# Kernel optimization log

Hardware: AMD Instinct MI355X
Metric: run time of the kernel (lower is better)

Reference implementation:

```python
import jax, jax.numpy as jnp
import numpy as np

B, N, K = 4, 4096, 16
D_POINTS, D_MODEL = 64, 128


def setup_inputs() -> dict:
    key = jax.random.key(0)
    ks = jax.random.split(key, 18)
    rn = lambda k, shp, s=0.05: (jax.random.normal(k, shp, jnp.float32) * s)
    return {
        "xyz": jax.random.normal(ks[0], (B, N, 3), jnp.float32),
        "features": jax.random.normal(ks[1], (B, N, D_POINTS), jnp.float32),
        # fc_delta: Linear(3,d_model) -> ReLU -> Linear(d_model,d_model)
        "Wd1": rn(ks[2], (3, D_MODEL)), "bd1": rn(ks[3], (D_MODEL,)),
        "Wd2": rn(ks[4], (D_MODEL, D_MODEL)), "bd2": rn(ks[5], (D_MODEL,)),
        # fc1: Linear(d_points, d_model)
        "Wf1": rn(ks[6], (D_POINTS, D_MODEL)), "bf1": rn(ks[7], (D_MODEL,)),
        # w_qs / w_ks / w_vs: Linear(d_model, d_model, bias=False)
        "Wq": rn(ks[8], (D_MODEL, D_MODEL)),
        "Wk": rn(ks[9], (D_MODEL, D_MODEL)),
        "Wv": rn(ks[10], (D_MODEL, D_MODEL)),
        # fc_gamma: Linear(d_model,d_model) -> ReLU -> Linear(d_model,d_model)
        "Wg1": rn(ks[11], (D_MODEL, D_MODEL)), "bg1": rn(ks[12], (D_MODEL,)),
        "Wg2": rn(ks[13], (D_MODEL, D_MODEL)), "bg2": rn(ks[14], (D_MODEL,)),
        # fc2: Linear(d_model, d_points)
        "Wo": rn(ks[15], (D_MODEL, D_POINTS)), "bo": rn(ks[16], (D_POINTS,)),
    }


def reference(xyz, features, Wd1, bd1, Wd2, bd2, Wf1, bf1, Wq, Wk, Wv,
              Wg1, bg1, Wg2, bg2, Wo, bo):
    sq = jnp.sum(xyz * xyz, axis=-1)
    d2 = sq[:, :, None] + sq[:, None, :] - 2.0 * jnp.einsum('bnd,bmd->bnm', xyz, xyz)
    # argsort()[:, :, :k] == k smallest distances (self included)
    _, knn_idx = jax.lax.top_k(-d2, K)  # [B,N,K] int32

    gather = jax.vmap(lambda a, i: a[i])  # per-batch fancy gather along point axis
    knn_xyz = gather(xyz, knn_idx)                       # [B,N,K,3]
    rel = xyz[:, :, None, :] - knn_xyz                   # [B,N,K,3]
    pos_enc = jax.nn.relu(rel @ Wd1 + bd1) @ Wd2 + bd2   # [B,N,K,D]

    shortcut = features
    f = features @ Wf1 + bf1                             # [B,N,D]
    knn_f = gather(f, knn_idx)                           # [B,N,K,D]

    q = f @ Wq                                           # [B,N,D]
    k = knn_f @ Wk                                       # [B,N,K,D]
    v = knn_f @ Wv                                       # [B,N,K,D]

    attn = q[:, :, None, :] - k + pos_enc                # [B,N,K,D]
    attn = jax.nn.relu(attn @ Wg1 + bg1) @ Wg2 + bg2
    attn = jax.nn.softmax(attn / np.sqrt(D_MODEL).astype(np.float32), axis=-2)

    res = jnp.einsum('bnkf,bnkf->bnf', attn, v + pos_enc)  # [B,N,D]
    return res @ Wo + bo + shortcut                        # [B,N,d_points]
```

## Files before the change

kernel.cpp:

```cpp
#include <hip/hip_runtime.h>
#include <hip/hip_bf16.h>

#define NPTS 4096
#define BATCH 4
#define BN (BATCH * NPTS)
#define DMODEL 128
#define DPTS 64
#define KNBR 16
#define SWS 136
#define PBLK 8

typedef unsigned short u16;
typedef unsigned int u32;
typedef unsigned long long u64;
typedef short bh8 __attribute__((ext_vector_type(8)));
typedef float f32x4 __attribute__((ext_vector_type(4)));

__device__ __forceinline__ float bfu(u16 u) {
    union { u32 i; float f; } c; c.i = ((u32)u) << 16; return c.f;
}
__device__ __forceinline__ u16 f2u(float x) {
    u32 u = __float_as_uint(x);
    u32 r = u + 0x7FFFu + ((u >> 16) & 1u);
    return (u16)(r >> 16);
}
__device__ __forceinline__ u32 pack2(float a, float b) {
    return (u32)f2u(a) | ((u32)f2u(b) << 16);
}
__device__ __forceinline__ float ldr(const void* p, long i, int mode) {
    return mode == 0 ? bfu(((const u16*)p)[i]) : ((const float*)p)[i];
}
__device__ __forceinline__ void str(void* p, long i, float v, int mode) {
    if (mode == 0) ((u16*)p)[i] = f2u(v);
    else ((float*)p)[i] = v;
}
__device__ __forceinline__ int detect_mode(const void* Wq) {
    const u16* w = (const u16*)Wq;
    int lane = threadIdx.x & 63;
    int tot = 0;
#pragma unroll
    for (int r = 0; r < 4; ++r) {
        unsigned e = (w[lane + r * 64] >> 7) & 0xFFu;
        bool wild = (e >= 132u) || (e > 0u && e <= 90u);
        tot += (int)__popcll(__ballot(wild));
    }
    return tot > 32 ? 1 : 0;
}

__global__ __launch_bounds__(256) void prep_kernel(
    const void* __restrict__ Wd2, const void* __restrict__ Wg1, const void* __restrict__ Wg2,
    const void* __restrict__ Wo, const void* __restrict__ Wq, const void* __restrict__ Wk,
    const void* __restrict__ Wv, const void* __restrict__ Wf1, const void* __restrict__ xyz,
    u16* __restrict__ WdT2, u16* __restrict__ WgT1, u16* __restrict__ WgT2,
    u16* __restrict__ WoT, u16* __restrict__ WqT, u16* __restrict__ WkT,
    u16* __restrict__ WvT, u16* __restrict__ WfT, float4* __restrict__ cloudF) {
    int mode = detect_mode(Wq);
    int gid = blockIdx.x * 256 + threadIdx.x;
    if (gid < 6 * 16384) {
        int m = gid >> 14, o = gid & 16383;
        int n = o >> 7, i = o & 127;
        const void* W = (m == 0) ? Wd2 : (m == 1) ? Wg1 : (m == 2) ? Wg2
                      : (m == 3) ? Wq  : (m == 4) ? Wk  : Wv;
        u16* D = (m == 0) ? WdT2 : (m == 1) ? WgT1 : (m == 2) ? WgT2
               : (m == 3) ? WqT  : (m == 4) ? WkT  : WvT;
        D[o] = f2u(ldr(W, (long)i * 128 + n, mode));
    } else if (gid < 6 * 16384 + 8192) {
        int o = gid - 6 * 16384;
        int n = o >> 6, k2 = o & 63;
        WfT[o] = f2u(ldr(Wf1, (long)k2 * 128 + n, mode));
    } else if (gid < 6 * 16384 + 16384) {
        int o2 = gid - 6 * 16384 - 8192;
        int col = o2 >> 7, i = o2 & 127;
        WoT[o2] = f2u(ldr(Wo, (long)i * 64 + col, mode));
    } else if (gid < 6 * 16384 + 16384 + 16384) {
        int i = gid - (6 * 16384 + 16384);
        float gx = ldr(xyz, (long)i * 3 + 0, mode);
        float gy = ldr(xyz, (long)i * 3 + 1, mode);
        float gz = ldr(xyz, (long)i * 3 + 2, mode);
        float4 f;
        f.x = gx; f.y = gy; f.z = gz;
        f.w = gx * gx + gy * gy + gz * gz;
        cloudF[i] = f;
    }
}

__global__ __launch_bounds__(256) void qkv_kernel(
    const void* __restrict__ feat, const void* __restrict__ bf1v, const void* __restrict__ WqRaw,
    const u16* __restrict__ WfT, const u16* __restrict__ WqT,
    const u16* __restrict__ WkT, const u16* __restrict__ WvT,
    u16* __restrict__ qw, u16* __restrict__ kfw, u16* __restrict__ vfw) {
    int mode = detect_mode(WqRaw);
    __shared__ __align__(16) u16 sFeat[64 * 72];
    __shared__ __align__(16) u16 sF[64 * SWS];
    const int t = threadIdx.x;
    const int p0 = blockIdx.x * 64;
    const int lane = t & 63, w = t >> 6;
    const int rg = (w & 1) * 32, cg = (w >> 1) * 64;
    const int lm = lane & 15, lq = lane >> 4;

    for (int i = t; i < 512; i += 256) {
        int r = i >> 3, c8 = i & 7;
        u16 tmp[8];
        if (mode == 0) {
            *(uint4*)tmp = *((const uint4*)feat + (long)(p0 + r) * 8 + c8);
        } else {
            const float* fp = (const float*)feat + (long)(p0 + r) * 64 + c8 * 8;
#pragma unroll
            for (int u = 0; u < 8; ++u) tmp[u] = f2u(fp[u]);
        }
        *(uint4*)(sFeat + r * 72 + c8 * 8) = *(uint4*)tmp;
    }
    __syncthreads();

    {
        f32x4 acc[2][4];
#pragma unroll
        for (int rt = 0; rt < 2; ++rt)
#pragma unroll
            for (int ct = 0; ct < 4; ++ct) { acc[rt][ct][0]=0.f; acc[rt][ct][1]=0.f; acc[rt][ct][2]=0.f; acc[rt][ct][3]=0.f; }
#pragma unroll
        for (int kk = 0; kk < 2; ++kk) {
            const int ko = kk * 32 + lq * 8;
            bh8 a0 = *(const bh8*)(sFeat + (rg + lm) * 72 + ko);
            bh8 a1 = *(const bh8*)(sFeat + (rg + 16 + lm) * 72 + ko);
            bh8 bq[4];
#pragma unroll
            for (int ct = 0; ct < 4; ++ct)
                bq[ct] = *(const bh8*)(WfT + (long)(cg + ct * 16 + lm) * 64 + ko);
#pragma unroll
            for (int ct = 0; ct < 4; ++ct) {
                acc[0][ct] = __builtin_amdgcn_mfma_f32_16x16x32_bf16(a0, bq[ct], acc[0][ct], 0, 0, 0);
                acc[1][ct] = __builtin_amdgcn_mfma_f32_16x16x32_bf16(a1, bq[ct], acc[1][ct], 0, 0, 0);
            }
        }
#pragma unroll
        for (int rt = 0; rt < 2; ++rt)
#pragma unroll
            for (int ct = 0; ct < 4; ++ct) {
                const int col = cg + ct * 16 + lm;
                const float bj = ldr(bf1v, col, mode);
#pragma unroll
                for (int r4 = 0; r4 < 4; ++r4) {
                    int row = rg + rt * 16 + lq * 4 + r4;
                    u32 u = (u32)f2u(acc[rt][ct][r4] + bj);
                    u32 o = __shfl_xor(u, 1);
                    if ((lane & 1) == 0)
                        *(u32*)(sF + row * SWS + col) = u | (o << 16);
                }
            }
    }
    __syncthreads();

    {
        const int m = blockIdx.y;
        const u16* Wm = (m == 0) ? WqT : (m == 1) ? WkT : WvT;
        u16* Om = (m == 0) ? qw : (m == 1) ? kfw : vfw;
        f32x4 acc[2][4];
#pragma unroll
        for (int rt = 0; rt < 2; ++rt)
#pragma unroll
            for (int ct = 0; ct < 4; ++ct) { acc[rt][ct][0]=0.f; acc[rt][ct][1]=0.f; acc[rt][ct][2]=0.f; acc[rt][ct][3]=0.f; }
#pragma unroll
        for (int kk = 0; kk < 4; ++kk) {
            const int ko = kk * 32 + lq * 8;
            bh8 a0 = *(const bh8*)(sF + (rg + lm) * SWS + ko);
            bh8 a1 = *(const bh8*)(sF + (rg + 16 + lm) * SWS + ko);
            bh8 bq[4];
#pragma unroll
            for (int ct = 0; ct < 4; ++ct)
                bq[ct] = *(const bh8*)(Wm + (long)(cg + ct * 16 + lm) * 128 + ko);
#pragma unroll
            for (int ct = 0; ct < 4; ++ct) {
                acc[0][ct] = __builtin_amdgcn_mfma_f32_16x16x32_bf16(a0, bq[ct], acc[0][ct], 0, 0, 0);
                acc[1][ct] = __builtin_amdgcn_mfma_f32_16x16x32_bf16(a1, bq[ct], acc[1][ct], 0, 0, 0);
            }
        }
#pragma unroll
        for (int rt = 0; rt < 2; ++rt)
#pragma unroll
            for (int ct = 0; ct < 4; ++ct) {
                const int col = cg + ct * 16 + lm;
#pragma unroll
                for (int r4 = 0; r4 < 4; ++r4) {
                    int row = rg + rt * 16 + lq * 4 + r4;
                    u32 u = (u32)f2u(acc[rt][ct][r4]);
                    u32 o = __shfl_xor(u, 1);
                    if ((lane & 1) == 0)
                        *(u32*)(Om + (long)(p0 + row) * DMODEL + col) = u | (o << 16);
                }
            }
    }
}

__global__ __launch_bounds__(256) void knn_kernel(
    const float4* __restrict__ cloudF, int* __restrict__ knnIdx) {
    const int t = threadIdx.x, lane = t & 63, w = t >> 6;
    const int p0 = blockIdx.x * 4;
    const long bbase = (long)(p0 >> 12) * NPTS;
    const float4* cl = cloudF + bbase;

    const int pl = (p0 & (NPTS - 1)) + w;
    float4 qv = cl[pl];
    const float m2x = -2.f * qv.x, m2y = -2.f * qv.y, m2z = -2.f * qv.z;

    u64 kv;
    {
        float4 c = cl[lane];
        float key = fmaf(m2x, c.x, fmaf(m2y, c.y, fmaf(m2z, c.z, c.w)));
        u32 uk = __float_as_uint(key);
        uk ^= (u32)((int)uk >> 31) | 0x80000000u;
        kv = ((u64)uk << 32) | (u32)lane;
#pragma unroll
        for (int k = 2; k <= 64; k <<= 1) {
#pragma unroll
            for (int j = k >> 1; j > 0; j >>= 1) {
                u64 other = __shfl_xor(kv, j);
                bool keepMin = ((lane & j) == 0) == ((lane & k) == 0);
                bool smaller = kv < other;
                kv = (keepMin == smaller) ? kv : other;
            }
        }
    }
    u32 Tu = __builtin_amdgcn_readlane((u32)(kv >> 32), 15);

    float4 cd0 = cl[64 + lane];
    float4 cd1 = cl[128 + lane];
#pragma unroll 1
    for (int it = 0; it < 32; ++it) {
        const int base = 64 + it * 128;
        float4 c0 = cd0, c1 = cd1;
        if (it < 31) {
            int n0 = base + 128 + lane;
            int n1 = n0 + 64 > 4095 ? 4095 : n0 + 64;
            cd0 = cl[n0];
            cd1 = cl[n1];
        }
        float k0 = fmaf(m2x, c0.x, fmaf(m2y, c0.y, fmaf(m2z, c0.z, c0.w)));
        float k1 = fmaf(m2x, c1.x, fmaf(m2y, c1.y, fmaf(m2z, c1.z, c1.w)));
        u32 u0 = __float_as_uint(k0); u0 ^= (u32)((int)u0 >> 31) | 0x80000000u;
        u32 u1 = __float_as_uint(k1); u1 ^= (u32)((int)u1 >> 31) | 0x80000000u;
        if (it == 31) u1 = 0xFFFFFFFFu;
        u32 umin = (u0 < u1) ? u0 : u1;
        unsigned long long mask = __ballot(umin < Tu);
        while (mask) {
            int l = __ffsll(mask) - 1;
            mask &= mask - 1;
            u32 a0 = __builtin_amdgcn_readlane(u0, l);
            u32 a1 = __builtin_amdgcn_readlane(u1, l);
            if (a0 < Tu) {
                u64 cand = ((u64)a0 << 32) | (u32)(base + l);
                u64 prev = __shfl_up(kv, 1);
                if (lane == 0) prev = 0;
                kv = (prev > cand) ? prev : ((kv > cand) ? cand : kv);
                Tu = __builtin_amdgcn_readlane((u32)(kv >> 32), 15);
            }
            if (a1 < Tu) {
                u64 cand = ((u64)a1 << 32) | (u32)(base + 64 + l);
                u64 prev = __shfl_up(kv, 1);
                if (lane == 0) prev = 0;
                kv = (prev > cand) ? prev : ((kv > cand) ? cand : kv);
                Tu = __builtin_amdgcn_readlane((u32)(kv >> 32), 15);
            }
        }
    }
    if (lane < 16) knnIdx[(long)(p0 + w) * 16 + lane] = (int)(u32)kv;
}

__device__ __forceinline__ void mfma8(const u16* sIn, const u16* __restrict__ Bg,
                                      const float* bias, bool dorelu, bool inplace,
                                      u16* sOut, int t) {
    const int lane = t & 63, w = t >> 6;
    const int rg = (w & 3) * 32, cg = (w >> 2) * 64;
    const int lm = lane & 15, lq = lane >> 4;
    f32x4 acc[2][4];
#pragma unroll
    for (int rt = 0; rt < 2; ++rt)
#pragma unroll
        for (int ct = 0; ct < 4; ++ct) { acc[rt][ct][0]=0.f; acc[rt][ct][1]=0.f; acc[rt][ct][2]=0.f; acc[rt][ct][3]=0.f; }
#pragma unroll
    for (int kk = 0; kk < 4; ++kk) {
        const int ko = kk * 32 + lq * 8;
        bh8 a0 = *(const bh8*)(sIn + (rg + lm) * SWS + ko);
        bh8 a1 = *(const bh8*)(sIn + (rg + 16 + lm) * SWS + ko);
        bh8 bq[4];
#pragma unroll
        for (int ct = 0; ct < 4; ++ct)
            bq[ct] = *(const bh8*)(Bg + (long)(cg + ct * 16 + lm) * 128 + ko);
#pragma unroll
        for (int ct = 0; ct < 4; ++ct) {
            acc[0][ct] = __builtin_amdgcn_mfma_f32_16x16x32_bf16(a0, bq[ct], acc[0][ct], 0, 0, 0);
            acc[1][ct] = __builtin_amdgcn_mfma_f32_16x16x32_bf16(a1, bq[ct], acc[1][ct], 0, 0, 0);
        }
    }
    if (inplace) __syncthreads();
#pragma unroll
    for (int rt = 0; rt < 2; ++rt)
#pragma unroll
        for (int ct = 0; ct < 4; ++ct) {
            const int col = cg + ct * 16 + lm;
            const float bj = bias[col];
#pragma unroll
            for (int r4 = 0; r4 < 4; ++r4) {
                int row = rg + rt * 16 + lq * 4 + r4;
                float v = acc[rt][ct][r4] + bj;
                if (dorelu) v = fmaxf(v, 0.f);
                u32 u = (u32)f2u(v);
                u32 o = __shfl_xor(u, 1);
                if ((lane & 1) == 0)
                    *(u32*)(sOut + row * SWS + col) = u | (o << 16);
            }
        }
}

#define ATT_SA 0
#define ATT_SPE 34816
#define ATT_SREL 69632
#define ATT_SBIAS 71680
#define ATT_SQ 73216
#define SMEM_BYTES 75264

__global__ __launch_bounds__(512, 4) void fused_kernel(
    const float4* __restrict__ cloudF, const int* __restrict__ knnIdx,
    const void* __restrict__ feat,
    const void* __restrict__ Wd1, const void* __restrict__ bd1, const void* __restrict__ bd2,
    const void* __restrict__ bg1, const void* __restrict__ bg2, const void* __restrict__ bo,
    const void* __restrict__ WqRaw,
    const u16* __restrict__ WdT2, const u16* __restrict__ WgT1, const u16* __restrict__ WgT2,
    const u16* __restrict__ WoT,
    const u16* __restrict__ qw, const u16* __restrict__ kfw, const u16* __restrict__ vfw,
    void* __restrict__ out) {
    int mode = detect_mode(WqRaw);
    __shared__ __align__(16) char smem[SMEM_BYTES];
    __shared__ int sIdx[128];
    u16* sA   = (u16*)(smem + ATT_SA);
    u16* sPE  = (u16*)(smem + ATT_SPE);
    float (*sRel)[4] = (float(*)[4])(smem + ATT_SREL);
    float* sBias = (float*)(smem + ATT_SBIAS);
    u16* sQ   = (u16*)(smem + ATT_SQ);

    const int t = threadIdx.x, lane = t & 63, w = t >> 6;
    const int lm = lane & 15, lq = lane >> 4;
    const int p0 = blockIdx.x * PBLK;
    const long bbase = (long)(p0 >> 12) * NPTS;
    const float4* cl = cloudF + bbase;

    for (int i = t; i < 384; i += 512) {
        const void* b = (i < 128) ? bd2 : (i < 256) ? bg1 : bg2;
        sBias[i] = ldr(b, i & 127, mode);
    }
    ((u32*)sQ)[t] = ((const u32*)(qw + (long)p0 * DMODEL))[t];
    const int ch = 2 * lane;
    const float wd0a = ldr(Wd1, ch, mode),       wd0b = ldr(Wd1, ch + 1, mode);
    const float wd1a = ldr(Wd1, 128 + ch, mode), wd1b = ldr(Wd1, 128 + ch + 1, mode);
    const float wd2a = ldr(Wd1, 256 + ch, mode), wd2b = ldr(Wd1, 256 + ch + 1, mode);
    const float bd1a = ldr(bd1, ch, mode),       bd1b = ldr(bd1, ch + 1, mode);
    if (t < 128) {
        int idx = knnIdx[(long)p0 * 16 + t];
        sIdx[t] = idx;
        int pl2 = (p0 & (NPTS - 1)) + (t >> 4);
        float4 pv = cl[pl2];
        float4 nv = cl[idx];
        sRel[t][0] = pv.x - nv.x;
        sRel[t][1] = pv.y - nv.y;
        sRel[t][2] = pv.z - nv.z;
    }
    __syncthreads();

#pragma unroll
    for (int i = 0; i < 16; ++i) {
        int r = w * 16 + i;
        float4 rl = *(const float4*)sRel[r];
        float h0 = fmaxf(bd1a + rl.x * wd0a + rl.y * wd1a + rl.z * wd2a, 0.f);
        float h1 = fmaxf(bd1b + rl.x * wd0b + rl.y * wd1b + rl.z * wd2b, 0.f);
        *(u32*)(sA + r * SWS + ch) = pack2(h0, h1);
    }
    __syncthreads();
    mfma8(sA, WdT2, sBias, false, false, sPE, t);
    __syncthreads();

#pragma unroll
    for (int i = 0; i < 16; ++i) {
        int r = w * 16 + i;
        u32 kv2 = *(const u32*)(kfw + (bbase + sIdx[r]) * (long)DMODEL + ch);
        u32 qv2 = *(const u32*)(sQ + (r >> 4) * DMODEL + ch);
        u32 pe2 = *(const u32*)(sPE + r * SWS + ch);
        float a0 = bfu((u16)qv2) - bfu((u16)kv2) + bfu((u16)pe2);
        float a1 = bfu((u16)(qv2 >> 16)) - bfu((u16)(kv2 >> 16)) + bfu((u16)(pe2 >> 16));
        *(u32*)(sA + r * SWS + ch) = pack2(a0, a1);
    }
    __syncthreads();
    mfma8(sA, WgT1, sBias + 128, true, true, sA, t);
    __syncthreads();
    mfma8(sA, WgT2, sBias + 256, false, true, sA, t);
    __syncthreads();

    float res0, res1;
    {
        float mx0 = -3e38f, mx1 = -3e38f;
#pragma unroll
        for (int k = 0; k < KNBR; ++k) {
            u32 l2 = *(const u32*)(sA + (w * 16 + k) * SWS + ch);
            mx0 = fmaxf(mx0, bfu((u16)l2));
            mx1 = fmaxf(mx1, bfu((u16)(l2 >> 16)));
        }
        const float inv = 0.08838834764831845f;
        float s0 = 0.f, s1 = 0.f, r0 = 0.f, r1 = 0.f;
#pragma unroll
        for (int k = 0; k < KNBR; ++k) {
            u32 l2 = *(const u32*)(sA + (w * 16 + k) * SWS + ch);
            u32 v2 = *(const u32*)(vfw + (bbase + sIdx[w * 16 + k]) * (long)DMODEL + ch);
            u32 p2 = *(const u32*)(sPE + (w * 16 + k) * SWS + ch);
            float e0 = __expf((bfu((u16)l2) - mx0) * inv);
            float e1 = __expf((bfu((u16)(l2 >> 16)) - mx1) * inv);
            s0 += e0; s1 += e1;
            r0 += e0 * (bfu((u16)v2) + bfu((u16)p2));
            r1 += e1 * (bfu((u16)(v2 >> 16)) + bfu((u16)(p2 >> 16)));
        }
        res0 = r0 / s0; res1 = r1 / s1;
    }
    __syncthreads();
    *(u32*)(sA + w * SWS + ch) = pack2(res0, res1);
    __syncthreads();

    if (w < 4) {
        const int col = w * 16 + lm;
        f32x4 acc = {0.f, 0.f, 0.f, 0.f};
#pragma unroll
        for (int kk = 0; kk < 4; ++kk) {
            const int ko = kk * 32 + lq * 8;
            bh8 aa = *(const bh8*)(sA + lm * SWS + ko);
            bh8 bb = *(const bh8*)(WoT + (long)col * DMODEL + ko);
            acc = __builtin_amdgcn_mfma_f32_16x16x32_bf16(aa, bb, acc, 0, 0, 0);
        }
        if (lq < 2) {
            float bov = ldr(bo, col, mode);
#pragma unroll
            for (int r4 = 0; r4 < 4; ++r4) {
                long p = p0 + lq * 4 + r4;
                float v = acc[r4] + bov + ldr(feat, p * DPTS + col, mode);
                str(out, p * DPTS + col, v, mode);
            }
        }
    }
}

extern "C" void kernel_launch(void* const* d_in, const int* in_sizes, int n_in,
                              void* d_out, int out_size, void* d_ws, size_t ws_size,
                              hipStream_t stream) {
    (void)in_sizes; (void)n_in; (void)out_size; (void)ws_size;
    char* ws = (char*)d_ws;
    u16* qw   = (u16*)(ws + 256);
    u16* kfw  = qw + (long)BN * DMODEL;
    u16* vfw  = kfw + (long)BN * DMODEL;
    u16* WdT2 = vfw + (long)BN * DMODEL;
    u16* WgT1 = WdT2 + 16384;
    u16* WgT2 = WgT1 + 16384;
    u16* WoT  = WgT2 + 16384;
    u16* WqT  = WoT + 8192;
    u16* WkT  = WqT + 16384;
    u16* WvT  = WkT + 16384;
    u16* WfT  = WvT + 16384;
    float4* cloudF = (float4*)(WfT + 8192);
    int* knnIdx = (int*)(cloudF + BN);

    prep_kernel<<<512, 256, 0, stream>>>(d_in[4], d_in[11], d_in[13], d_in[15],
                                         d_in[8], d_in[9], d_in[10], d_in[6], d_in[0],
                                         WdT2, WgT1, WgT2, WoT, WqT, WkT, WvT, WfT,
                                         cloudF);
    qkv_kernel<<<dim3(BN / 64, 3), 256, 0, stream>>>(d_in[1], d_in[7], d_in[8],
                                                     WfT, WqT, WkT, WvT, qw, kfw, vfw);
    knn_kernel<<<BN / 4, 256, 0, stream>>>(cloudF, knnIdx);
    fused_kernel<<<BN / PBLK, 512, 0, stream>>>(cloudF, knnIdx, d_in[1],
                                                d_in[2], d_in[3], d_in[5],
                                                d_in[12], d_in[14], d_in[16], d_in[8],
                                                WdT2, WgT1, WgT2, WoT,
                                                qw, kfw, vfw, d_out);
}
```

Baseline: 301.6 us.

## Merge QKV and kNN kernels into one launch and prefetch gathered K/V rows

The QKV projection and kNN search kernels become a single launch, with block index choosing which role a block runs, so the two independent workloads can share the GPU concurrently and one launch boundary disappears. In the fused attention kernel, the gathered key rows are loaded into registers before the positional-encoding MFMA, and the value rows before the gamma MLP MFMAs. This lets those global gathers overlap with compute instead of sitting on the critical path. The cost is more register pressure in the fused kernel and a shared-memory footprint in the merged kernel that kNN blocks reserve even though they may not use it, which could lower occupancy.

```diff
diff --git a/kernel.cpp b/kernel.cpp
--- a/kernel.cpp
+++ b/kernel.cpp
@@ -9,6 +9,7 @@
 #define KNBR 16
 #define SWS 136
 #define PBLK 8
+#define QKV_BLOCKS 768
 
 typedef unsigned short u16;
 typedef unsigned int u32;
@@ -84,118 +85,119 @@
     }
 }
 
-__global__ __launch_bounds__(256) void qkv_kernel(
+__global__ __launch_bounds__(256) void pre_kernel(
     const void* __restrict__ feat, const void* __restrict__ bf1v, const void* __restrict__ WqRaw,
     const u16* __restrict__ WfT, const u16* __restrict__ WqT,
     const u16* __restrict__ WkT, const u16* __restrict__ WvT,
-    u16* __restrict__ qw, u16* __restrict__ kfw, u16* __restrict__ vfw) {
-    int mode = detect_mode(WqRaw);
+    u16* __restrict__ qw, u16* __restrict__ kfw, u16* __restrict__ vfw,
+    const float4* __restrict__ cloudF, int* __restrict__ knnIdx) {
     __shared__ __align__(16) u16 sFeat[64 * 72];
     __shared__ __align__(16) u16 sF[64 * SWS];
     const int t = threadIdx.x;
-    const int p0 = blockIdx.x * 64;
     const int lane = t & 63, w = t >> 6;
-    const int rg = (w & 1) * 32, cg = (w >> 1) * 64;
-    const int lm = lane & 15, lq = lane >> 4;
-
-    for (int i = t; i < 512; i += 256) {
-        int r = i >> 3, c8 = i & 7;
-        u16 tmp[8];
-        if (mode == 0) {
-            *(uint4*)tmp = *((const uint4*)feat + (long)(p0 + r) * 8 + c8);
-        } else {
-            const float* fp = (const float*)feat + (long)(p0 + r) * 64 + c8 * 8;
-#pragma unroll
-            for (int u = 0; u < 8; ++u) tmp[u] = f2u(fp[u]);
-        }
-        *(uint4*)(sFeat + r * 72 + c8 * 8) = *(uint4*)tmp;
-    }
-    __syncthreads();
-
-    {
-        f32x4 acc[2][4];
-#pragma unroll
-        for (int rt = 0; rt < 2; ++rt)
-#pragma unroll
-            for (int ct = 0; ct < 4; ++ct) { acc[rt][ct][0]=0.f; acc[rt][ct][1]=0.f; acc[rt][ct][2]=0.f; acc[rt][ct][3]=0.f; }
-#pragma unroll
-        for (int kk = 0; kk < 2; ++kk) {
-            const int ko = kk * 32 + lq * 8;
-            bh8 a0 = *(const bh8*)(sFeat + (rg + lm) * 72 + ko);
-            bh8 a1 = *(const bh8*)(sFeat + (rg + 16 + lm) * 72 + ko);
-            bh8 bq[4];
-#pragma unroll
-            for (int ct = 0; ct < 4; ++ct)
-                bq[ct] = *(const bh8*)(WfT + (long)(cg + ct * 16 + lm) * 64 + ko);
-#pragma unroll
-            for (int ct = 0; ct < 4; ++ct) {
-                acc[0][ct] = __builtin_amdgcn_mfma_f32_16x16x32_bf16(a0, bq[ct], acc[0][ct], 0, 0, 0);
-                acc[1][ct] = __builtin_amdgcn_mfma_f32_16x16x32_bf16(a1, bq[ct], acc[1][ct], 0, 0, 0);
-            }
-        }
-#pragma unroll
-        for (int rt = 0; rt < 2; ++rt)
-#pragma unroll
-            for (int ct = 0; ct < 4; ++ct) {
-                const int col = cg + ct * 16 + lm;
-                const float bj = ldr(bf1v, col, mode);
-#pragma unroll
-                for (int r4 = 0; r4 < 4; ++r4) {
-                    int row = rg + rt * 16 + lq * 4 + r4;
-                    u32 u = (u32)f2u(acc[rt][ct][r4] + bj);
-                    u32 o = __shfl_xor(u, 1);
-                    if ((lane & 1) == 0)
-                        *(u32*)(sF + row * SWS + col) = u | (o << 16);
+
+    if (blockIdx.x < QKV_BLOCKS) {
+        int mode = detect_mode(WqRaw);
+        const int p0 = (blockIdx.x & 255) * 64;
+        const int m = blockIdx.x >> 8;
+        const int rg = (w & 1) * 32, cg = (w >> 1) * 64;
+        const int lm = lane & 15, lq = lane >> 4;
+
+        for (int i = t; i < 512; i += 256) {
+            int r = i >> 3, c8 = i & 7;
+            u16 tmp[8];
+            if (mode == 0) {
+                *(uint4*)tmp = *((const uint4*)feat + (long)(p0 + r) * 8 + c8);
+            } else {
+                const float* fp = (const float*)feat + (long)(p0 + r) * 64 + c8 * 8;
+#pragma unroll
+                for (int u = 0; u < 8; ++u) tmp[u] = f2u(fp[u]);
+            }
+            *(uint4*)(sFeat + r * 72 + c8 * 8) = *(uint4*)tmp;
+        }
+        __syncthreads();
+
+        {
+            f32x4 acc[2][4];
+#pragma unroll
+            for (int rt = 0; rt < 2; ++rt)
+#pragma unroll
+                for (int ct = 0; ct < 4; ++ct) { acc[rt][ct][0]=0.f; acc[rt][ct][1]=0.f; acc[rt][ct][2]=0.f; acc[rt][ct][3]=0.f; }
+#pragma unroll
+            for (int kk = 0; kk < 2; ++kk) {
+                const int ko = kk * 32 + lq * 8;
+                bh8 a0 = *(const bh8*)(sFeat + (rg + lm) * 72 + ko);
+                bh8 a1 = *(const bh8*)(sFeat + (rg + 16 + lm) * 72 + ko);
+                bh8 bq[4];
+#pragma unroll
+                for (int ct = 0; ct < 4; ++ct)
+                    bq[ct] = *(const bh8*)(WfT + (long)(cg + ct * 16 + lm) * 64 + ko);
+#pragma unroll
+                for (int ct = 0; ct < 4; ++ct) {
+                    acc[0][ct] = __builtin_amdgcn_mfma_f32_16x16x32_bf16(a0, bq[ct], acc[0][ct], 0, 0, 0);
+                    acc[1][ct] = __builtin_amdgcn_mfma_f32_16x16x32_bf16(a1, bq[ct], acc[1][ct], 0, 0, 0);
                 }
             }
-    }
-    __syncthreads();
-
-    {
-        const int m = blockIdx.y;
-        const u16* Wm = (m == 0) ? WqT : (m == 1) ? WkT : WvT;
-        u16* Om = (m == 0) ? qw : (m == 1) ? kfw : vfw;
-        f32x4 acc[2][4];
-#pragma unroll
-        for (int rt = 0; rt < 2; ++rt)
-#pragma unroll
-            for (int ct = 0; ct < 4; ++ct) { acc[rt][ct][0]=0.f; acc[rt][ct][1]=0.f; acc[rt][ct][2]=0.f; acc[rt][ct][3]=0.f; }
-#pragma unroll
-        for (int kk = 0; kk < 4; ++kk) {
-            const int ko = kk * 32 + lq * 8;
-            bh8 a0 = *(const bh8*)(sF + (rg + lm) * SWS + ko);
-            bh8 a1 = *(const bh8*)(sF + (rg + 16 + lm) * SWS + ko);
-            bh8 bq[4];
-#pragma unroll
-            for (int ct = 0; ct < 4; ++ct)
-                bq[ct] = *(const bh8*)(Wm + (long)(cg + ct * 16 + lm) * 128 + ko);
-#pragma unroll
-            for (int ct = 0; ct < 4; ++ct) {
-                acc[0][ct] = __builtin_amdgcn_mfma_f32_16x16x32_bf16(a0, bq[ct], acc[0][ct], 0, 0, 0);
-                acc[1][ct] = __builtin_amdgcn_mfma_f32_16x16x32_bf16(a1, bq[ct], acc[1][ct], 0, 0, 0);
-            }
-        }
-#pragma unroll
-        for (int rt = 0; rt < 2; ++rt)
-#pragma unroll
-            for (int ct = 0; ct < 4; ++ct) {
-                const int col = cg + ct * 16 + lm;
-#pragma unroll
-                for (int r4 = 0; r4 < 4; ++r4) {
-                    int row = rg + rt * 16 + lq * 4 + r4;
-                    u32 u = (u32)f2u(acc[rt][ct][r4]);
-                    u32 o = __shfl_xor(u, 1);
-                    if ((lane & 1) == 0)
-                        *(u32*)(Om + (long)(p0 + row) * DMODEL + col) = u | (o << 16);
+#pragma unroll
+            for (int rt = 0; rt < 2; ++rt)
+#pragma unroll
+                for (int ct = 0; ct < 4; ++ct) {
+                    const int col = cg + ct * 16 + lm;
+                    const float bj = ldr(bf1v, col, mode);
+#pragma unroll
+                    for (int r4 = 0; r4 < 4; ++r4) {
+                        int row = rg + rt * 16 + lq * 4 + r4;
+                        u32 u = (u32)f2u(acc[rt][ct][r4] + bj);
+                        u32 o = __shfl_xor(u, 1);
+                        if ((lane & 1) == 0)
+                            *(u32*)(sF + row * SWS + col) = u | (o << 16);
+                    }
                 }
-            }
-    }
-}
-
-__global__ __launch_bounds__(256) void knn_kernel(
-    const float4* __restrict__ cloudF, int* __restrict__ knnIdx) {
-    const int t = threadIdx.x, lane = t & 63, w = t >> 6;
-    const int p0 = blockIdx.x * 4;
+        }
+        __syncthreads();
+
+        {
+            const u16* Wm = (m == 0) ? WqT : (m == 1) ? WkT : WvT;
+            u16* Om = (m == 0) ? qw : (m == 1) ? kfw : vfw;
+            f32x4 acc[2][4];
+#pragma unroll
+            for (int rt = 0; rt < 2; ++rt)
+#pragma unroll
+                for (int ct = 0; ct < 4; ++ct) { acc[rt][ct][0]=0.f; acc[rt][ct][1]=0.f; acc[rt][ct][2]=0.f; acc[rt][ct][3]=0.f; }
+#pragma unroll
+            for (int kk = 0; kk < 4; ++kk) {
+                const int ko = kk * 32 + lq * 8;
+                bh8 a0 = *(const bh8*)(sF + (rg + lm) * SWS + ko);
+                bh8 a1 = *(const bh8*)(sF + (rg + 16 + lm) * SWS + ko);
+                bh8 bq[4];
+#pragma unroll
+                for (int ct = 0; ct < 4; ++ct)
+                    bq[ct] = *(const bh8*)(Wm + (long)(cg + ct * 16 + lm) * 128 + ko);
+#pragma unroll
+                for (int ct = 0; ct < 4; ++ct) {
+                    acc[0][ct] = __builtin_amdgcn_mfma_f32_16x16x32_bf16(a0, bq[ct], acc[0][ct], 0, 0, 0);
+                    acc[1][ct] = __builtin_amdgcn_mfma_f32_16x16x32_bf16(a1, bq[ct], acc[1][ct], 0, 0, 0);
+                }
+            }
+#pragma unroll
+            for (int rt = 0; rt < 2; ++rt)
+#pragma unroll
+                for (int ct = 0; ct < 4; ++ct) {
+                    const int col = cg + ct * 16 + lm;
+#pragma unroll
+                    for (int r4 = 0; r4 < 4; ++r4) {
+                        int row = rg + rt * 16 + lq * 4 + r4;
+                        u32 u = (u32)f2u(acc[rt][ct][r4]);
+                        u32 o = __shfl_xor(u, 1);
+                        if ((lane & 1) == 0)
+                            *(u32*)(Om + (long)(p0 + row) * DMODEL + col) = u | (o << 16);
+                    }
+                }
+        }
+        return;
+    }
+
+    const int p0 = (blockIdx.x - QKV_BLOCKS) * 4;
     const long bbase = (long)(p0 >> 12) * NPTS;
     const float4* cl = cloudF + bbase;
 
@@ -366,6 +368,11 @@
     }
     __syncthreads();
 
+    u32 kf2[16];
+#pragma unroll
+    for (int i = 0; i < 16; ++i)
+        kf2[i] = *(const u32*)(kfw + (bbase + sIdx[w * 16 + i]) * (long)DMODEL + ch);
+
 #pragma unroll
     for (int i = 0; i < 16; ++i) {
         int r = w * 16 + i;
@@ -378,17 +385,25 @@
     mfma8(sA, WdT2, sBias, false, false, sPE, t);
     __syncthreads();
 
-#pragma unroll
-    for (int i = 0; i < 16; ++i) {
-        int r = w * 16 + i;
-        u32 kv2 = *(const u32*)(kfw + (bbase + sIdx[r]) * (long)DMODEL + ch);
-        u32 qv2 = *(const u32*)(sQ + (r >> 4) * DMODEL + ch);
-        u32 pe2 = *(const u32*)(sPE + r * SWS + ch);
-        float a0 = bfu((u16)qv2) - bfu((u16)kv2) + bfu((u16)pe2);
-        float a1 = bfu((u16)(qv2 >> 16)) - bfu((u16)(kv2 >> 16)) + bfu((u16)(pe2 >> 16));
-        *(u32*)(sA + r * SWS + ch) = pack2(a0, a1);
-    }
-    __syncthreads();
+    {
+        const u32 qv2 = *(const u32*)(sQ + w * DMODEL + ch);
+#pragma unroll
+        for (int i = 0; i < 16; ++i) {
+            int r = w * 16 + i;
+            u32 kv2 = kf2[i];
+            u32 pe2 = *(const u32*)(sPE + r * SWS + ch);
+            float a0 = bfu((u16)qv2) - bfu((u16)kv2) + bfu((u16)pe2);
+            float a1 = bfu((u16)(qv2 >> 16)) - bfu((u16)(kv2 >> 16)) + bfu((u16)(pe2 >> 16));
+            *(u32*)(sA + r * SWS + ch) = pack2(a0, a1);
+        }
+    }
+    __syncthreads();
+
+    u32 vv2[16];
+#pragma unroll
+    for (int k = 0; k < KNBR; ++k)
+        vv2[k] = *(const u32*)(vfw + (bbase + sIdx[w * 16 + k]) * (long)DMODEL + ch);
+
     mfma8(sA, WgT1, sBias + 128, true, true, sA, t);
     __syncthreads();
     mfma8(sA, WgT2, sBias + 256, false, true, sA, t);
@@ -408,7 +423,7 @@
 #pragma unroll
         for (int k = 0; k < KNBR; ++k) {
             u32 l2 = *(const u32*)(sA + (w * 16 + k) * SWS + ch);
-            u32 v2 = *(const u32*)(vfw + (bbase + sIdx[w * 16 + k]) * (long)DMODEL + ch);
+            u32 v2 = vv2[k];
             u32 p2 = *(const u32*)(sPE + (w * 16 + k) * SWS + ch);
             float e0 = __expf((bfu((u16)l2) - mx0) * inv);
             float e1 = __expf((bfu((u16)(l2 >> 16)) - mx1) * inv);
@@ -467,9 +482,9 @@
                                          d_in[8], d_in[9], d_in[10], d_in[6], d_in[0],
                                          WdT2, WgT1, WgT2, WoT, WqT, WkT, WvT, WfT,
                                          cloudF);
-    qkv_kernel<<<dim3(BN / 64, 3), 256, 0, stream>>>(d_in[1], d_in[7], d_in[8],
-                                                     WfT, WqT, WkT, WvT, qw, kfw, vfw);
-    knn_kernel<<<BN / 4, 256, 0, stream>>>(cloudF, knnIdx);
+    pre_kernel<<<QKV_BLOCKS + BN / 4, 256, 0, stream>>>(d_in[1], d_in[7], d_in[8],
+                                                        WfT, WqT, WkT, WvT,
+                                                        qw, kfw, vfw, cloudF, knnIdx);
     fused_kernel<<<BN / PBLK, 512, 0, stream>>>(cloudF, knnIdx, d_in[1],
                                                 d_in[2], d_in[3], d_in[5],
                                                 d_in[12], d_in[14], d_in[16], d_in[8],
```

Result: no change. 306.6 us (+1.6%).

## Split kNN scan across four waves per query and fuse PE epilogue

Applied to the files above, without the earlier changes.

The kNN kernel now gives each query point a whole block: four waves each scan a quarter of the cloud and keep a local top-16, then one wave merges the 64 candidates with a bitonic sort. This shortens the serial per-query scan at the cost of four times more blocks and an extra merge step. Separately, the fused kernel computes the positional-encoding matmul inline and builds q-k+pe straight from the accumulators, dropping one LDS round trip and one barrier. The catch is that the k-feature gather now happens in a scattered per-element pattern.

```diff
diff --git a/kernel.cpp b/kernel.cpp
--- a/kernel.cpp
+++ b/kernel.cpp
@@ -194,22 +194,24 @@
 
 __global__ __launch_bounds__(256) void knn_kernel(
     const float4* __restrict__ cloudF, int* __restrict__ knnIdx) {
+    __shared__ u64 sM[64];
     const int t = threadIdx.x, lane = t & 63, w = t >> 6;
-    const int p0 = blockIdx.x * 4;
-    const long bbase = (long)(p0 >> 12) * NPTS;
+    const int pp = blockIdx.x;
+    const long bbase = (long)(pp >> 12) * NPTS;
     const float4* cl = cloudF + bbase;
 
-    const int pl = (p0 & (NPTS - 1)) + w;
+    const int pl = pp & (NPTS - 1);
     float4 qv = cl[pl];
     const float m2x = -2.f * qv.x, m2y = -2.f * qv.y, m2z = -2.f * qv.z;
+    const int base0 = w * 1024;
 
     u64 kv;
     {
-        float4 c = cl[lane];
+        float4 c = cl[base0 + lane];
         float key = fmaf(m2x, c.x, fmaf(m2y, c.y, fmaf(m2z, c.z, c.w)));
         u32 uk = __float_as_uint(key);
         uk ^= (u32)((int)uk >> 31) | 0x80000000u;
-        kv = ((u64)uk << 32) | (u32)lane;
+        kv = ((u64)uk << 32) | (u32)(base0 + lane);
 #pragma unroll
         for (int k = 2; k <= 64; k <<= 1) {
 #pragma unroll
@@ -223,15 +225,15 @@
     }
     u32 Tu = __builtin_amdgcn_readlane((u32)(kv >> 32), 15);
 
-    float4 cd0 = cl[64 + lane];
-    float4 cd1 = cl[128 + lane];
+    float4 cd0 = cl[base0 + 64 + lane];
+    float4 cd1 = cl[base0 + 128 + lane];
 #pragma unroll 1
-    for (int it = 0; it < 32; ++it) {
-        const int base = 64 + it * 128;
+    for (int it = 0; it < 8; ++it) {
+        const int base = base0 + 64 + it * 128;
         float4 c0 = cd0, c1 = cd1;
-        if (it < 31) {
+        if (it < 7) {
             int n0 = base + 128 + lane;
-            int n1 = n0 + 64 > 4095 ? 4095 : n0 + 64;
+            int n1 = n0 + 64 > base0 + 1023 ? base0 + 1023 : n0 + 64;
             cd0 = cl[n0];
             cd1 = cl[n1];
         }
@@ -239,7 +241,7 @@
         float k1 = fmaf(m2x, c1.x, fmaf(m2y, c1.y, fmaf(m2z, c1.z, c1.w)));
         u32 u0 = __float_as_uint(k0); u0 ^= (u32)((int)u0 >> 31) | 0x80000000u;
         u32 u1 = __float_as_uint(k1); u1 ^= (u32)((int)u1 >> 31) | 0x80000000u;
-        if (it == 31) u1 = 0xFFFFFFFFu;
+        if (it == 7) u1 = 0xFFFFFFFFu;
         u32 umin = (u0 < u1) ? u0 : u1;
         unsigned long long mask = __ballot(umin < Tu);
         while (mask) {
@@ -263,7 +265,23 @@
             }
         }
     }
-    if (lane < 16) knnIdx[(long)(p0 + w) * 16 + lane] = (int)(u32)kv;
+    if (lane < 16) sM[w * 16 + lane] = kv;
+    __syncthreads();
+
+    if (w == 0) {
+        u64 mv = sM[lane];
+#pragma unroll
+        for (int k = 2; k <= 64; k <<= 1) {
+#pragma unroll
+            for (int j = k >> 1; j > 0; j >>= 1) {
+                u64 other = __shfl_xor(mv, j);
+                bool keepMin = ((lane & j) == 0) == ((lane & k) == 0);
+                bool smaller = mv < other;
+                mv = (keepMin == smaller) ? mv : other;
+            }
+        }
+        if (lane < 16) knnIdx[(long)pp * 16 + lane] = (int)(u32)mv;
+    }
 }
 
 __device__ __forceinline__ void mfma8(const u16* sIn, const u16* __restrict__ Bg,
@@ -375,18 +393,51 @@
         *(u32*)(sA + r * SWS + ch) = pack2(h0, h1);
     }
     __syncthreads();
-    mfma8(sA, WdT2, sBias, false, false, sPE, t);
-    __syncthreads();
-
-#pragma unroll
-    for (int i = 0; i < 16; ++i) {
-        int r = w * 16 + i;
-        u32 kv2 = *(const u32*)(kfw + (bbase + sIdx[r]) * (long)DMODEL + ch);
-        u32 qv2 = *(const u32*)(sQ + (r >> 4) * DMODEL + ch);
-        u32 pe2 = *(const u32*)(sPE + r * SWS + ch);
-        float a0 = bfu((u16)qv2) - bfu((u16)kv2) + bfu((u16)pe2);
-        float a1 = bfu((u16)(qv2 >> 16)) - bfu((u16)(kv2 >> 16)) + bfu((u16)(pe2 >> 16));
-        *(u32*)(sA + r * SWS + ch) = pack2(a0, a1);
+
+    {
+        const int rg = (w & 3) * 32, cg = (w >> 2) * 64;
+        f32x4 acc[2][4];
+#pragma unroll
+        for (int rt = 0; rt < 2; ++rt)
+#pragma unroll
+            for (int ct = 0; ct < 4; ++ct) { acc[rt][ct][0]=0.f; acc[rt][ct][1]=0.f; acc[rt][ct][2]=0.f; acc[rt][ct][3]=0.f; }
+#pragma unroll
+        for (int kk = 0; kk < 4; ++kk) {
+            const int ko = kk * 32 + lq * 8;
+            bh8 a0 = *(const bh8*)(sA + (rg + lm) * SWS + ko);
+            bh8 a1 = *(const bh8*)(sA + (rg + 16 + lm) * SWS + ko);
+            bh8 bq[4];
+#pragma unroll
+            for (int ct = 0; ct < 4; ++ct)
+                bq[ct] = *(const bh8*)(WdT2 + (long)(cg + ct * 16 + lm) * 128 + ko);
+#pragma unroll
+            for (int ct = 0; ct < 4; ++ct) {
+                acc[0][ct] = __builtin_amdgcn_mfma_f32_16x16x32_bf16(a0, bq[ct], acc[0][ct], 0, 0, 0);
+                acc[1][ct] = __builtin_amdgcn_mfma_f32_16x16x32_bf16(a1, bq[ct], acc[1][ct], 0, 0, 0);
+            }
+        }
+        __syncthreads();
+#pragma unroll
+        for (int rt = 0; rt < 2; ++rt)
+#pragma unroll
+            for (int ct = 0; ct < 4; ++ct) {
+                const int col = cg + ct * 16 + lm;
+                const float bj = sBias[col];
+                const int pt = (w & 3) * 2 + rt;
+                const float qvf = bfu(sQ[pt * DMODEL + col]);
+#pragma unroll
+                for (int r4 = 0; r4 < 4; ++r4) {
+                    int row = rg + rt * 16 + lq * 4 + r4;
+                    float pev = acc[rt][ct][r4] + bj;
+                    float av = qvf - bfu(kfw[(bbase + sIdx[row]) * (long)DMODEL + col]) + pev;
+                    u32 up = (u32)f2u(pev); u32 op = __shfl_xor(up, 1);
+                    u32 ua = (u32)f2u(av);  u32 oa = __shfl_xor(ua, 1);
+                    if ((lane & 1) == 0) {
+                        *(u32*)(sPE + row * SWS + col) = up | (op << 16);
+                        *(u32*)(sA  + row * SWS + col) = ua | (oa << 16);
+                    }
+                }
+            }
     }
     __syncthreads();
     mfma8(sA, WgT1, sBias + 128, true, true, sA, t);
@@ -469,7 +520,7 @@
                                          cloudF);
     qkv_kernel<<<dim3(BN / 64, 3), 256, 0, stream>>>(d_in[1], d_in[7], d_in[8],
                                                      WfT, WqT, WkT, WvT, qw, kfw, vfw);
-    knn_kernel<<<BN / 4, 256, 0, stream>>>(cloudF, knnIdx);
+    knn_kernel<<<BN, 256, 0, stream>>>(cloudF, knnIdx);
     fused_kernel<<<BN / PBLK, 512, 0, stream>>>(cloudF, knnIdx, d_in[1],
                                                 d_in[2], d_in[3], d_in[5],
                                                 d_in[12], d_in[14], d_in[16], d_in[8],
```

Measured after the change: 378.0 us. 1.25x slower.
